# Kernel optimization log

Measured on AMD Instinct MI355X. Metric: run time of the kernel, lower is better.

The kernel has to match this reference:

```python
import jax, jax.numpy as jnp
import numpy as np

B, V, C, D, H, W = 2, 3, 32, 48, 128, 160


def _bilinear_sample(img, x, y):
    # img: [C,H,W]; x,y: [N] pixel coords; zero padding outside the image
    Ci, Hi, Wi = img.shape
    x0 = jnp.floor(x); y0 = jnp.floor(y)
    x1 = x0 + 1.0; y1 = y0 + 1.0
    wx1 = x - x0; wx0 = 1.0 - wx1
    wy1 = y - y0; wy0 = 1.0 - wy1

    def gather(xi, yi):
        valid = (xi >= 0) & (xi <= Wi - 1) & (yi >= 0) & (yi <= Hi - 1)
        xc = jnp.clip(xi, 0, Wi - 1).astype(jnp.int32)
        yc = jnp.clip(yi, 0, Hi - 1).astype(jnp.int32)
        return img[:, yc, xc] * valid.astype(img.dtype)  # [C,N]

    return (gather(x0, y0) * (wx0 * wy0) + gather(x1, y0) * (wx1 * wy0)
            + gather(x0, y1) * (wx0 * wy1) + gather(x1, y1) * (wx1 * wy1))


def homo_warping(src_fea, src_proj, ref_proj, depth_values):
    # src_fea [B,C,H,W], projs [B,4,4], depth_values [B,D] -> [B,C,D,H,W]
    Bn, Cn, Hn, Wn = src_fea.shape
    Dn = depth_values.shape[1]
    proj = src_proj @ jnp.linalg.inv(ref_proj)          # [B,4,4]
    rot = proj[:, :3, :3]
    trans = proj[:, :3, 3]
    ys, xs = jnp.meshgrid(jnp.arange(Hn, dtype=src_fea.dtype),
                          jnp.arange(Wn, dtype=src_fea.dtype), indexing='ij')
    xyz = jnp.stack([xs.ravel(), ys.ravel(), jnp.ones(Hn * Wn, src_fea.dtype)])  # [3,HW]
    rot_xyz = jnp.einsum('bij,jn->bin', rot, xyz)       # [B,3,HW]
    pts = rot_xyz[:, :, None, :] * depth_values[:, None, :, None] \
          + trans[:, :, None, None]                     # [B,3,D,HW]
    z = pts[:, 2]
    z = jnp.where(jnp.abs(z) < 1e-6, 1e-6, z)
    px = (pts[:, 0] / z).reshape(Bn, -1)                # [B,D*HW]
    py = (pts[:, 1] / z).reshape(Bn, -1)
    warped = jax.vmap(_bilinear_sample)(src_fea, px, py)  # [B,C,D*HW]
    return warped.reshape(Bn, Cn, Dn, Hn, Wn)


def setup_inputs():
    key = jax.random.key(0)
    k1, k2 = jax.random.split(key)
    features = jax.random.normal(k1, (V, B, C, H, W), jnp.float32)
    # realistic pinhole projection matrices K @ [R|t] (4x4)
    f = 300.0
    K = np.array([[f, 0, W / 2, 0], [0, f, H / 2, 0],
                  [0, 0, 1, 0], [0, 0, 0, 1]], np.float32)
    projs = []
    for v in range(V):
        E = np.eye(4, dtype=np.float32)
        E[0, 3] = 2.0 * v   # small camera baseline
        E[1, 3] = -1.0 * v
        projs.append(K @ E)
    proj_matrices = jnp.asarray(np.broadcast_to(np.stack(projs), (B, V, 4, 4)).copy())
    depth_values = jnp.tile(jnp.linspace(425.0, 935.0, D, dtype=jnp.float32)[None], (B, 1))
    reg_w = jax.random.normal(k2, (1, C, 3, 3, 3), jnp.float32) * 0.05
    reg_b = jnp.zeros((1,), jnp.float32)
    return {"features": features, "proj_matrices": proj_matrices,
            "depth_values": depth_values, "num_depth": D,
            "reg_w": reg_w, "reg_b": reg_b}


def reference(features, proj_matrices, depth_values, num_depth, reg_w, reg_b):
    num_views = features.shape[0]
    ref_feature = features[0]                         # [B,C,H,W]
    ref_proj = proj_matrices[:, 0]
    Bn, Cn, Hn, Wn = ref_feature.shape
    ref_volume = jnp.broadcast_to(ref_feature[:, :, None], (Bn, Cn, num_depth, Hn, Wn))
    volume_sum = ref_volume
    volume_sq_sum = ref_volume ** 2
    for v in range(1, num_views):
        wv = homo_warping(features[v], proj_matrices[:, v], ref_proj, depth_values)
        volume_sum = volume_sum + wv
        volume_sq_sum = volume_sq_sum + wv * wv
    variance = volume_sq_sum / num_views - (volume_sum / num_views) ** 2
    # cost regularization: Conv3d(C->1, k=3, pad=1)
    cost = jax.lax.conv_general_dilated(
        variance, reg_w, (1, 1, 1), [(1, 1), (1, 1), (1, 1)],
        dimension_numbers=('NCDHW', 'OIDHW', 'NCDHW'))
    cost = cost + reg_b[None, :, None, None, None]
    prob = jax.nn.softmax(cost[:, 0], axis=1)         # [B,D,H,W]
    depth = jnp.sum(prob * depth_values[:, :, None, None], axis=1)  # [B,H,W]
    # photometric confidence: sum over 4 consecutive depth probs (== 4*avg_pool3d)
    psum4 = jax.lax.reduce_window(prob, 0.0, jax.lax.add, (1, 4, 1, 1), (1, 1, 1, 1),
                                  [(0, 0), (1, 2), (0, 0), (0, 0)])
    didx = jnp.sum(prob * jnp.arange(num_depth, dtype=prob.dtype)[None, :, None, None], axis=1)
    didx = jnp.clip(didx.astype(jnp.int32), 0, num_depth - 1)
    conf = jnp.take_along_axis(psum4, didx[:, None], axis=1)[:, 0]
    return depth, conf
```

## Files before the change

### kernel.cpp

```cpp
#include <hip/hip_runtime.h>
#include <hip/hip_bf16.h>
#include <hip/hip_fp16.h>

#define Hh 128
#define Ww 160
#define Cc 32
#define Dd 48
#define Bb 2
#define Vv 3
#define HW (Hh*Ww)
#define VS 40

typedef _Float16 f16x8 __attribute__((ext_vector_type(8)));
typedef float f32x4 __attribute__((ext_vector_type(4)));

__global__ void k_proj(const float* __restrict__ pm, const float* __restrict__ wt,
                       float* __restrict__ P, ushort* __restrict__ Bfr) {
    int t = threadIdx.x;
    if (t < Bb * (Vv - 1)) {
        int b = t >> 1;
        int v = (t & 1) + 1;
        const float* ref = pm + (b * Vv + 0) * 16;
        const float* src = pm + (b * Vv + v) * 16;
        float A[4][8];
        for (int i = 0; i < 4; ++i)
            for (int j = 0; j < 4; ++j) {
                A[i][j] = ref[i * 4 + j];
                A[i][4 + j] = (i == j) ? 1.0f : 0.0f;
            }
        for (int col = 0; col < 4; ++col) {
            int piv = col;
            for (int r = col + 1; r < 4; ++r)
                if (fabsf(A[r][col]) > fabsf(A[piv][col])) piv = r;
            if (piv != col)
                for (int j = 0; j < 8; ++j) { float tmp = A[col][j]; A[col][j] = A[piv][j]; A[piv][j] = tmp; }
            float inv = 1.0f / A[col][col];
            for (int j = 0; j < 8; ++j) A[col][j] *= inv;
            for (int r = 0; r < 4; ++r) {
                if (r == col) continue;
                float f = A[r][col];
                for (int j = 0; j < 8; ++j) A[r][j] -= f * A[col][j];
            }
        }
        float Pm[3][4];
        for (int i = 0; i < 3; ++i)
            for (int j = 0; j < 4; ++j) {
                float s = 0.f;
                for (int k = 0; k < 4; ++k) s += src[i * 4 + k] * A[k][4 + j];
                Pm[i][j] = s;
            }
        float* o = P + t * 12;
        o[0] = Pm[0][0]; o[1] = Pm[0][1]; o[2] = Pm[0][2];
        o[3] = Pm[1][0]; o[4] = Pm[1][1]; o[5] = Pm[1][2];
        o[6] = Pm[2][0]; o[7] = Pm[2][1]; o[8] = Pm[2][2];
        o[9] = Pm[0][3]; o[10] = Pm[1][3]; o[11] = Pm[2][3];
    }
    int kd = t & 15, q = t >> 4;
    for (int tap = 0; tap < 9; ++tap) {
        ushort* dst = Bfr + (tap * 64 + t) * 8;
        for (int j = 0; j < 8; ++j) {
            float w = (kd < 3) ? wt[(q * 8 + j) * 27 + kd * 9 + tap] : 0.f;
            __half h = __float2half(w);
            dst[j] = *(ushort*)&h;
        }
    }
}

__global__ void k_transpose(const float* __restrict__ f, ushort* __restrict__ featT) {
    __shared__ float t[Cc][Ww + 1];
    int slice = blockIdx.x;
    int vb = slice / Hh, y = slice % Hh;
    const float* src = f + (size_t)vb * Cc * HW + (size_t)y * Ww;
    ushort* dst = featT + ((size_t)vb * Hh + y) * Ww * Cc;
    for (int i = threadIdx.x; i < Cc * Ww; i += 256) {
        int c = i / Ww, x = i - c * Ww;
        t[c][x] = src[(size_t)c * HW + x];
    }
    __syncthreads();
    for (int i = threadIdx.x; i < Ww * 4; i += 256) {
        int x = i >> 2, c8 = i & 3;
        union { uint4 u; ushort s[8]; } pk;
#pragma unroll
        for (int j = 0; j < 8; ++j) {
            __half h = __float2half(t[c8 * 8 + j][x]);
            pk.s[j] = *(ushort*)&h;
        }
        *(uint4*)&dst[x * Cc + c8 * 8] = pk.u;
    }
}

__global__ __launch_bounds__(256, 4)
void k_main(const ushort* __restrict__ featT, const float* __restrict__ P,
            const float* __restrict__ dvals, const ushort* __restrict__ Bfr,
            float* __restrict__ S) {
    __shared__ ushort vsh[324 * VS];
    __shared__ unsigned int offs[324 * 4];
    __shared__ unsigned int wgts[324 * 4];
    __shared__ float rt[24];
    const int tid = threadIdx.x;
    const int b = blockIdx.z, d = blockIdx.y;
    const int tileY = blockIdx.x / 10, tileX = blockIdx.x - (blockIdx.x / 10) * 10;

    if (tid < 24) rt[tid] = P[b * 24 + tid];
    const float depth = dvals[b * Dd + d];
    __syncthreads();

#pragma unroll 1
    for (int p = tid; p < 324; p += 256) {
        int pyt = p / 18, pxt = p - pyt * 18;
        int gy = tileY * 16 + pyt - 1, gx = tileX * 16 + pxt - 1;
        if ((unsigned)gy >= (unsigned)Hh || (unsigned)gx >= (unsigned)Ww) continue;
#pragma unroll
        for (int vi = 0; vi < 2; ++vi) {
            const float* M = &rt[vi * 12];
            float fgx = (float)gx, fgy = (float)gy;
            float rx = M[0] * fgx + M[1] * fgy + M[2];
            float ry = M[3] * fgx + M[4] * fgy + M[5];
            float rz = M[6] * fgx + M[7] * fgy + M[8];
            float X = rx * depth + M[9];
            float Y = ry * depth + M[10];
            float Z = rz * depth + M[11];
            float z = (fabsf(Z) < 1e-6f) ? 1e-6f : Z;
            float u = X / z, vv = Y / z;
            float x0f = floorf(u), y0f = floorf(vv);
            float fx = u - x0f, fy = vv - y0f;
            int x0 = (int)x0f, y0 = (int)y0f;
            int x1 = x0 + 1, y1 = y0 + 1;
            bool vx0 = (x0 >= 0) && (x0 <= Ww - 1);
            bool vx1 = (x1 >= 0) && (x1 <= Ww - 1);
            bool vy0 = (y0 >= 0) && (y0 <= Hh - 1);
            bool vy1 = (y1 >= 0) && (y1 <= Hh - 1);
            int xc0 = min(max(x0, 0), Ww - 1), xc1 = min(max(x1, 0), Ww - 1);
            int yc0 = min(max(y0, 0), Hh - 1), yc1 = min(max(y1, 0), Hh - 1);
            unsigned int p00 = (unsigned)(yc0 * Ww + xc0);
            unsigned int p01 = (unsigned)(yc0 * Ww + xc1);
            unsigned int p10 = (unsigned)(yc1 * Ww + xc0);
            unsigned int p11 = (unsigned)(yc1 * Ww + xc1);
            float w0 = (vx0 && vy0) ? (1.f - fx) * (1.f - fy) : 0.f;
            float w1 = (vx1 && vy0) ? fx * (1.f - fy) : 0.f;
            float w2 = (vx0 && vy1) ? (1.f - fx) * fy : 0.f;
            float w3 = (vx1 && vy1) ? fx * fy : 0.f;
            offs[p * 4 + vi * 2 + 0] = p00 | (p01 << 16);
            offs[p * 4 + vi * 2 + 1] = p10 | (p11 << 16);
            __half2 ha = __floats2half2_rn(w0, w1);
            __half2 hb = __floats2half2_rn(w2, w3);
            wgts[p * 4 + vi * 2 + 0] = *(unsigned int*)&ha;
            wgts[p * 4 + vi * 2 + 1] = *(unsigned int*)&hb;
        }
    }
    __syncthreads();

    const ushort* b1 = featT + (size_t)(1 * Bb + b) * HW * Cc;
    const ushort* b2 = featT + (size_t)(2 * Bb + b) * HW * Cc;
    const ushort* br = featT + (size_t)b * HW * Cc;

#pragma unroll 1
    for (int i = tid; i < 1296; i += 256) {
        int p = i >> 2, c8 = i & 3;
        int pyt = p / 18, pxt = p - pyt * 18;
        int gy = tileY * 16 + pyt - 1, gx = tileX * 16 + pxt - 1;
        ushort* dst = &vsh[p * VS + c8 * 8];
        if ((unsigned)gy >= (unsigned)Hh || (unsigned)gx >= (unsigned)Ww) {
            *(uint4*)dst = make_uint4(0u, 0u, 0u, 0u);
            continue;
        }
        uint4 oo = *(const uint4*)&offs[p * 4];
        uint4 wwp = *(const uint4*)&wgts[p * 4];
        int cb = c8 * 8;
        int o00 = (int)(oo.x & 0xffffu) * Cc + cb;
        int o01 = (int)(oo.x >> 16)     * Cc + cb;
        int o10 = (int)(oo.y & 0xffffu) * Cc + cb;
        int o11 = (int)(oo.y >> 16)     * Cc + cb;
        int o20 = (int)(oo.z & 0xffffu) * Cc + cb;
        int o21 = (int)(oo.z >> 16)     * Cc + cb;
        int o30 = (int)(oo.w & 0xffffu) * Cc + cb;
        int o31 = (int)(oo.w >> 16)     * Cc + cb;
        __half2 hv0 = *(__half2*)&wwp.x;
        __half2 hv1 = *(__half2*)&wwp.y;
        __half2 hv2 = *(__half2*)&wwp.z;
        __half2 hv3 = *(__half2*)&wwp.w;
        __half2 w00 = __half2half2(__low2half(hv0)), w01 = __half2half2(__high2half(hv0));
        __half2 w02 = __half2half2(__low2half(hv1)), w03 = __half2half2(__high2half(hv1));
        __half2 w10 = __half2half2(__low2half(hv2)), w11 = __half2half2(__high2half(hv2));
        __half2 w12 = __half2half2(__low2half(hv3)), w13 = __half2half2(__high2half(hv3));
        union U { uint4 u; __half2 h[4]; };
        U R, C0, C1, C2, C3, E0, E1, E2, E3, V;
        R.u  = *(const uint4*)(br + (size_t)(gy * Ww + gx) * Cc + cb);
        C0.u = *(const uint4*)(b1 + o00);
        C1.u = *(const uint4*)(b1 + o01);
        C2.u = *(const uint4*)(b1 + o10);
        C3.u = *(const uint4*)(b1 + o11);
        E0.u = *(const uint4*)(b2 + o20);
        E1.u = *(const uint4*)(b2 + o21);
        E2.u = *(const uint4*)(b2 + o30);
        E3.u = *(const uint4*)(b2 + o31);
        const __half2 third2 = __float2half2_rn(1.0f / 3.0f);
#pragma unroll
        for (int k = 0; k < 4; ++k) {
            __half2 s1 = __hmul2(w00, C0.h[k]);
            s1 = __hfma2(w01, C1.h[k], s1);
            s1 = __hfma2(w02, C2.h[k], s1);
            s1 = __hfma2(w03, C3.h[k], s1);
            __half2 s2 = __hmul2(w10, E0.h[k]);
            s2 = __hfma2(w11, E1.h[k], s2);
            s2 = __hfma2(w12, E2.h[k], s2);
            s2 = __hfma2(w13, E3.h[k], s2);
            __half2 r = R.h[k];
            __half2 sum = __hadd2(__hadd2(r, s1), s2);
            __half2 sq = __hmul2(r, r);
            sq = __hfma2(s1, s1, sq);
            sq = __hfma2(s2, s2, sq);
            __half2 m = __hmul2(sum, third2);
            __half2 var = __hfma2(__hneg2(m), m, __hmul2(sq, third2));
            V.h[k] = var;
        }
        *(uint4*)dst = V.u;
    }
    __syncthreads();

    const int lane = tid & 63;
    const int wave = tid >> 6;
    const int q = lane >> 4;
    const int n = lane & 15;
#pragma unroll 1
    for (int rr = 0; rr < 4; ++rr) {
        int row = wave * 4 + rr;
        f32x4 acc = {0.f, 0.f, 0.f, 0.f};
#pragma unroll
        for (int tap = 0; tap < 9; ++tap) {
            int kh = tap / 3, kw = tap - 3 * (tap / 3);
            union { uint4 u; f16x8 v; } A, Bf;
            A.u  = *(const uint4*)&vsh[((row + kh) * 18 + n + kw) * VS + q * 8];
            Bf.u = *(const uint4*)(Bfr + ((tap * 64 + lane) << 3));
            acc = __builtin_amdgcn_mfma_f32_16x16x32_f16(A.v, Bf.v, acc, 0, 0, 0);
        }
        if (n < 3) {
            int gy = tileY * 16 + row;
            int gxb = tileX * 16 + q * 4;
            float4 o = make_float4(acc[0], acc[1], acc[2], acc[3]);
            *(float4*)&S[((size_t)(b * 3 + n) * Dd + d) * HW + (size_t)gy * Ww + gxb] = o;
        }
    }
}

__global__ __launch_bounds__(256)
void k_post(const float* __restrict__ S, const float* __restrict__ dvals,
            float* __restrict__ out) {
    const int tid = threadIdx.x;
    const int lane = tid & 63, wave = tid >> 6;
    const int q = lane >> 4;
    const int pl = lane & 15;
    int pix_g = (blockIdx.x * 4 + wave) * 16 + pl;
    int b = pix_g / HW;
    int pix = pix_g - b * HW;
    const float* S0 = S + ((size_t)(b * 3 + 0) * Dd) * HW + pix;
    const float* S1 = S + ((size_t)(b * 3 + 1) * Dd) * HW + pix;
    const float* S2 = S + ((size_t)(b * 3 + 2) * Dd) * HW + pix;
    const int d0 = q * 12;
    float cost[12];
#pragma unroll
    for (int j = 0; j < 12; ++j) {
        int dd = d0 + j;
        float cst = S1[(size_t)dd * HW];
        if (dd > 0)      cst += S0[(size_t)(dd - 1) * HW];
        if (dd < Dd - 1) cst += S2[(size_t)(dd + 1) * HW];
        cost[j] = cst;
    }
    float m = cost[0];
#pragma unroll
    for (int j = 1; j < 12; ++j) m = fmaxf(m, cost[j]);
    m = fmaxf(m, __shfl_xor(m, 16));
    m = fmaxf(m, __shfl_xor(m, 32));
    float sum = 0.f, dep = 0.f, di = 0.f;
#pragma unroll
    for (int j = 0; j < 12; ++j) {
        float e = __expf(cost[j] - m);
        cost[j] = e;
        sum += e;
        dep += e * dvals[b * Dd + d0 + j];
        di  += e * (float)(d0 + j);
    }
    sum += __shfl_xor(sum, 16); sum += __shfl_xor(sum, 32);
    dep += __shfl_xor(dep, 16); dep += __shfl_xor(dep, 32);
    di  += __shfl_xor(di, 16);  di  += __shfl_xor(di, 32);
    float inv = 1.0f / sum;
    di *= inv;
    int didx = (int)di;
    didx = min(max(didx, 0), Dd - 1);
    float win = 0.f;
#pragma unroll
    for (int j = 0; j < 12; ++j) {
        int dd = d0 + j;
        win += ((dd >= didx - 1) && (dd <= didx + 2)) ? cost[j] : 0.f;
    }
    win += __shfl_xor(win, 16); win += __shfl_xor(win, 32);
    if (q == 0) {
        out[pix_g] = dep * inv;
        out[Bb * HW + pix_g] = win * inv;
    }
}

extern "C" void kernel_launch(void* const* d_in, const int* in_sizes, int n_in,
                              void* d_out, int out_size, void* d_ws, size_t ws_size,
                              hipStream_t stream) {
    const float* features = (const float*)d_in[0];
    const float* pm       = (const float*)d_in[1];
    const float* dvals    = (const float*)d_in[2];
    const float* reg_w    = (const float*)d_in[4];
    float* outp = (float*)d_out;

    char* ws = (char*)d_ws;
    ushort* featT = (ushort*)ws;
    size_t featT_bytes = (size_t)Vv * Bb * Hh * Ww * Cc * sizeof(ushort);
    float* P = (float*)(ws + featT_bytes);
    float* S = (float*)(ws + featT_bytes + 512);
    size_t S_bytes = (size_t)Bb * 3 * Dd * HW * sizeof(float);
    ushort* Bfr = (ushort*)(ws + featT_bytes + 512 + S_bytes);

    k_proj<<<1, 64, 0, stream>>>(pm, reg_w, P, Bfr);
    k_transpose<<<Vv * Bb * Hh, 256, 0, stream>>>(features, featT);
    k_main<<<dim3(80, Dd, Bb), 256, 0, stream>>>(featT, P, dvals, Bfr, S);
    k_post<<<(Bb * HW) / 64, 256, 0, stream>>>(S, dvals, outp);
}
```

Baseline: 155.0 us.

## Fuse projection setup into transpose, swizzle LDS volume, hoist MFMA weights to registers

Folds the single-block projection/weight-packing kernel into block 0 of the transpose kernel, removing one launch. The transpose now reads features with float4 loads. In k_main, the LDS variance tile drops its padding stride from 40 to 32 and uses an XOR swizzle of the 8-channel chunk to avoid bank conflicts, which also frees LDS. The B-fragment weights are preloaded once into registers instead of being reloaded per row, and launch bounds are raised to 5 blocks per SM. More live registers from the 9 hoisted uint4 fragments may conflict with the higher occupancy target and cause spills.

```diff
diff --git a/kernel.cpp b/kernel.cpp
--- a/kernel.cpp
+++ b/kernel.cpp
@@ -9,75 +9,76 @@
 #define Bb 2
 #define Vv 3
 #define HW (Hh*Ww)
-#define VS 40
+#define VS 32
 
 typedef _Float16 f16x8 __attribute__((ext_vector_type(8)));
 typedef float f32x4 __attribute__((ext_vector_type(4)));
 
-__global__ void k_proj(const float* __restrict__ pm, const float* __restrict__ wt,
-                       float* __restrict__ P, ushort* __restrict__ Bfr) {
-    int t = threadIdx.x;
-    if (t < Bb * (Vv - 1)) {
-        int b = t >> 1;
-        int v = (t & 1) + 1;
-        const float* ref = pm + (b * Vv + 0) * 16;
-        const float* src = pm + (b * Vv + v) * 16;
-        float A[4][8];
-        for (int i = 0; i < 4; ++i)
-            for (int j = 0; j < 4; ++j) {
-                A[i][j] = ref[i * 4 + j];
-                A[i][4 + j] = (i == j) ? 1.0f : 0.0f;
+__global__ void k_transpose(const float* __restrict__ f, const float* __restrict__ pm,
+                            const float* __restrict__ wt, ushort* __restrict__ featT,
+                            float* __restrict__ P, ushort* __restrict__ Bfr) {
+    __shared__ float t[Cc][Ww + 1];
+    const int tid = threadIdx.x;
+    if (blockIdx.x == 0 && tid < 64) {
+        if (tid < Bb * (Vv - 1)) {
+            int b = tid >> 1;
+            int v = (tid & 1) + 1;
+            const float* ref = pm + (b * Vv + 0) * 16;
+            const float* src = pm + (b * Vv + v) * 16;
+            float A[4][8];
+            for (int i = 0; i < 4; ++i)
+                for (int j = 0; j < 4; ++j) {
+                    A[i][j] = ref[i * 4 + j];
+                    A[i][4 + j] = (i == j) ? 1.0f : 0.0f;
+                }
+            for (int col = 0; col < 4; ++col) {
+                int piv = col;
+                for (int r = col + 1; r < 4; ++r)
+                    if (fabsf(A[r][col]) > fabsf(A[piv][col])) piv = r;
+                if (piv != col)
+                    for (int j = 0; j < 8; ++j) { float tmp = A[col][j]; A[col][j] = A[piv][j]; A[piv][j] = tmp; }
+                float inv = 1.0f / A[col][col];
+                for (int j = 0; j < 8; ++j) A[col][j] *= inv;
+                for (int r = 0; r < 4; ++r) {
+                    if (r == col) continue;
+                    float fct = A[r][col];
+                    for (int j = 0; j < 8; ++j) A[r][j] -= fct * A[col][j];
+                }
             }
-        for (int col = 0; col < 4; ++col) {
-            int piv = col;
-            for (int r = col + 1; r < 4; ++r)
-                if (fabsf(A[r][col]) > fabsf(A[piv][col])) piv = r;
-            if (piv != col)
-                for (int j = 0; j < 8; ++j) { float tmp = A[col][j]; A[col][j] = A[piv][j]; A[piv][j] = tmp; }
-            float inv = 1.0f / A[col][col];
-            for (int j = 0; j < 8; ++j) A[col][j] *= inv;
-            for (int r = 0; r < 4; ++r) {
-                if (r == col) continue;
-                float f = A[r][col];
-                for (int j = 0; j < 8; ++j) A[r][j] -= f * A[col][j];
+            float Pm[3][4];
+            for (int i = 0; i < 3; ++i)
+                for (int j = 0; j < 4; ++j) {
+                    float s = 0.f;
+                    for (int k = 0; k < 4; ++k) s += src[i * 4 + k] * A[k][4 + j];
+                    Pm[i][j] = s;
+                }
+            float* o = P + tid * 12;
+            o[0] = Pm[0][0]; o[1] = Pm[0][1]; o[2] = Pm[0][2];
+            o[3] = Pm[1][0]; o[4] = Pm[1][1]; o[5] = Pm[1][2];
+            o[6] = Pm[2][0]; o[7] = Pm[2][1]; o[8] = Pm[2][2];
+            o[9] = Pm[0][3]; o[10] = Pm[1][3]; o[11] = Pm[2][3];
+        }
+        int kd = tid & 15, q = tid >> 4;
+        for (int tap = 0; tap < 9; ++tap) {
+            ushort* dst = Bfr + (tap * 64 + tid) * 8;
+            for (int j = 0; j < 8; ++j) {
+                float w = (kd < 3) ? wt[(q * 8 + j) * 27 + kd * 9 + tap] : 0.f;
+                __half h = __float2half(w);
+                dst[j] = *(ushort*)&h;
             }
         }
-        float Pm[3][4];
-        for (int i = 0; i < 3; ++i)
-            for (int j = 0; j < 4; ++j) {
-                float s = 0.f;
-                for (int k = 0; k < 4; ++k) s += src[i * 4 + k] * A[k][4 + j];
-                Pm[i][j] = s;
-            }
-        float* o = P + t * 12;
-        o[0] = Pm[0][0]; o[1] = Pm[0][1]; o[2] = Pm[0][2];
-        o[3] = Pm[1][0]; o[4] = Pm[1][1]; o[5] = Pm[1][2];
-        o[6] = Pm[2][0]; o[7] = Pm[2][1]; o[8] = Pm[2][2];
-        o[9] = Pm[0][3]; o[10] = Pm[1][3]; o[11] = Pm[2][3];
-    }
-    int kd = t & 15, q = t >> 4;
-    for (int tap = 0; tap < 9; ++tap) {
-        ushort* dst = Bfr + (tap * 64 + t) * 8;
-        for (int j = 0; j < 8; ++j) {
-            float w = (kd < 3) ? wt[(q * 8 + j) * 27 + kd * 9 + tap] : 0.f;
-            __half h = __float2half(w);
-            dst[j] = *(ushort*)&h;
-        }
-    }
-}
-
-__global__ void k_transpose(const float* __restrict__ f, ushort* __restrict__ featT) {
-    __shared__ float t[Cc][Ww + 1];
+    }
     int slice = blockIdx.x;
     int vb = slice / Hh, y = slice % Hh;
     const float* src = f + (size_t)vb * Cc * HW + (size_t)y * Ww;
     ushort* dst = featT + ((size_t)vb * Hh + y) * Ww * Cc;
-    for (int i = threadIdx.x; i < Cc * Ww; i += 256) {
-        int c = i / Ww, x = i - c * Ww;
-        t[c][x] = src[(size_t)c * HW + x];
+    for (int i = tid; i < Cc * (Ww / 4); i += 256) {
+        int c = i / (Ww / 4), x4 = (i - c * (Ww / 4)) * 4;
+        float4 v = *(const float4*)(src + (size_t)c * HW + x4);
+        t[c][x4] = v.x; t[c][x4 + 1] = v.y; t[c][x4 + 2] = v.z; t[c][x4 + 3] = v.w;
     }
     __syncthreads();
-    for (int i = threadIdx.x; i < Ww * 4; i += 256) {
+    for (int i = tid; i < Ww * 4; i += 256) {
         int x = i >> 2, c8 = i & 3;
         union { uint4 u; ushort s[8]; } pk;
 #pragma unroll
@@ -89,7 +90,7 @@
     }
 }
 
-__global__ __launch_bounds__(256, 4)
+__global__ __launch_bounds__(256, 5)
 void k_main(const ushort* __restrict__ featT, const float* __restrict__ P,
             const float* __restrict__ dvals, const ushort* __restrict__ Bfr,
             float* __restrict__ S) {
@@ -159,7 +160,7 @@
         int p = i >> 2, c8 = i & 3;
         int pyt = p / 18, pxt = p - pyt * 18;
         int gy = tileY * 16 + pyt - 1, gx = tileX * 16 + pxt - 1;
-        ushort* dst = &vsh[p * VS + c8 * 8];
+        ushort* dst = &vsh[p * VS + (c8 ^ (p & 3)) * 8];
         if ((unsigned)gy >= (unsigned)Hh || (unsigned)gx >= (unsigned)Ww) {
             *(uint4*)dst = make_uint4(0u, 0u, 0u, 0u);
             continue;
@@ -222,6 +223,10 @@
     const int wave = tid >> 6;
     const int q = lane >> 4;
     const int n = lane & 15;
+    uint4 bf[9];
+#pragma unroll
+    for (int tap = 0; tap < 9; ++tap)
+        bf[tap] = *(const uint4*)(Bfr + ((tap * 64 + lane) << 3));
 #pragma unroll 1
     for (int rr = 0; rr < 4; ++rr) {
         int row = wave * 4 + rr;
@@ -229,9 +234,10 @@
 #pragma unroll
         for (int tap = 0; tap < 9; ++tap) {
             int kh = tap / 3, kw = tap - 3 * (tap / 3);
+            int slot = (row + kh) * 18 + n + kw;
             union { uint4 u; f16x8 v; } A, Bf;
-            A.u  = *(const uint4*)&vsh[((row + kh) * 18 + n + kw) * VS + q * 8];
-            Bf.u = *(const uint4*)(Bfr + ((tap * 64 + lane) << 3));
+            A.u  = *(const uint4*)&vsh[slot * VS + (q ^ (slot & 3)) * 8];
+            Bf.u = bf[tap];
             acc = __builtin_amdgcn_mfma_f32_16x16x32_f16(A.v, Bf.v, acc, 0, 0, 0);
         }
         if (n < 3) {
@@ -317,8 +323,7 @@
     size_t S_bytes = (size_t)Bb * 3 * Dd * HW * sizeof(float);
     ushort* Bfr = (ushort*)(ws + featT_bytes + 512 + S_bytes);
 
-    k_proj<<<1, 64, 0, stream>>>(pm, reg_w, P, Bfr);
-    k_transpose<<<Vv * Bb * Hh, 256, 0, stream>>>(features, featT);
+    k_transpose<<<Vv * Bb * Hh, 256, 0, stream>>>(features, pm, reg_w, featT, P, Bfr);
     k_main<<<dim3(80, Dd, Bb), 256, 0, stream>>>(featT, P, dvals, Bfr, S);
     k_post<<<(Bb * HW) / 64, 256, 0, stream>>>(S, dvals, outp);
 }
```

Result: no change. 152.6 us (-1.5%).
